# Optimization experiments

Measured on AMD Instinct MI355X. Metric: run time of the kernel, lower is better.

Reference implementation:

```python
import jax, jax.numpy as jnp
import numpy as np

D_MODEL = 256
NUM_HEADS = 8
DIM_HEAD = D_MODEL // NUM_HEADS
EPS = 1e-6
MASK_BIAS = -1.0e9


def setup_inputs() -> dict:
    key = jax.random.key(0)
    ks = jax.random.split(key, 10)
    B, S = 2, 4096
    x = jax.random.normal(ks[0], (B, S, D_MODEL), dtype=jnp.float32)
    pad_mask = jnp.zeros((B, S), dtype=jnp.float32)  # 1.0 => padded position
    scale = 1.0 / np.sqrt(D_MODEL)
    Wq = jax.random.normal(ks[1], (D_MODEL, D_MODEL), dtype=jnp.float32) * scale
    bq = jnp.zeros((D_MODEL,), dtype=jnp.float32)
    Wk = jax.random.normal(ks[2], (D_MODEL, D_MODEL), dtype=jnp.float32) * scale
    bk = jnp.zeros((D_MODEL,), dtype=jnp.float32)
    Wv = jax.random.normal(ks[3], (D_MODEL, D_MODEL), dtype=jnp.float32) * scale
    bv = jnp.zeros((D_MODEL,), dtype=jnp.float32)
    gamma = jnp.ones((D_MODEL,), dtype=jnp.float32)
    beta = jnp.zeros((D_MODEL,), dtype=jnp.float32)
    return {"x": x, "pad_mask": pad_mask, "Wq": Wq, "bq": bq, "Wk": Wk,
            "bk": bk, "Wv": Wv, "bv": bv, "gamma": gamma, "beta": beta}


def _layer_norm(h, gamma, beta):
    mu = jnp.mean(h, axis=-1, keepdims=True)
    var = jnp.mean(jnp.square(h - mu), axis=-1, keepdims=True)
    return gamma * (h - mu) * jax.lax.rsqrt(var + EPS) + beta


def reference(x, pad_mask, Wq, bq, Wk, bk, Wv, bv, gamma, beta):
    B, S, D = x.shape
    q = x @ Wq + bq  # [B,S,D]
    k = x @ Wk + bk
    v = x @ Wv + bv
    # split heads: [B,S,D] -> [B,H,S,Dh]
    def split(t):
        return t.reshape(B, S, NUM_HEADS, DIM_HEAD).transpose(0, 2, 1, 3)
    qh, kh, vh = split(q), split(k), split(v)
    w = jnp.einsum("bhqd,bhkd->bhqk", qh, kh)  # [B,H,S,S]
    # faithful to source: mask added BEFORE the 1/sqrt(dim_head) scaling
    w = w + pad_mask[:, None, None, :] * MASK_BIAS
    w = w / jnp.sqrt(jnp.float32(DIM_HEAD))
    attn = jax.nn.softmax(w, axis=-1)
    # dropout is identity at inference
    out = jnp.einsum("bhqk,bhkd->bhqd", attn, vh)  # [B,H,S,Dh]
    out = out.transpose(0, 2, 1, 3).reshape(B, S, D)
    return _layer_norm(out + x, gamma, beta)
```

## Files before the change

kernel.cpp:

```cpp
#include <hip/hip_runtime.h>
#include <hip/hip_bf16.h>

#define D_MODEL 256
#define NUM_HEADS 8
#define DIM_HEAD 32
#define SEQ 4096
#define BATCH 2
#define NROWS (BATCH * SEQ)
#define LN_EPS 1e-6f
#define MASK_BIAS -1.0e9f
#define SCALE 0.17677669529663687f
#define LOG2E 1.4426950408889634f
#define QSCALE (SCALE * LOG2E)

typedef __attribute__((ext_vector_type(8))) short short8;
typedef __attribute__((ext_vector_type(4))) float f32x4;

static __device__ __forceinline__ unsigned short f2b(float f) {
    union { __hip_bfloat16 b; unsigned short u; } cv;
    cv.b = __float2bfloat16(f);
    return cv.u;
}
static __device__ __forceinline__ unsigned int pk_bf16(float lo, float hi) {
    union { __hip_bfloat162 v; unsigned int u; } cv;
    cv.v = __float22bfloat162_rn(make_float2(lo, hi));
    return cv.u;
}
static __device__ __forceinline__ float exp2_raw(float x) {
#if __has_builtin(__builtin_amdgcn_exp2f)
    return __builtin_amdgcn_exp2f(x);
#else
    float r;
    asm volatile("v_exp_f32 %0, %1" : "=v"(r) : "v"(x));
    return r;
#endif
}
static __device__ __forceinline__ void load_lds16(const void* g, void* l) {
    __builtin_amdgcn_global_load_lds(
        (const __attribute__((address_space(1))) unsigned int*)g,
        (__attribute__((address_space(3))) unsigned int*)l, 16, 0, 0);
}

__global__ __launch_bounds__(256) void prep_kernel(
    const float* __restrict__ Wq, const float* __restrict__ Wk,
    const float* __restrict__ Wv,
    const float* __restrict__ bq, const float* __restrict__ bk,
    const float* __restrict__ bv,
    const float* __restrict__ pad,
    unsigned short* __restrict__ Wt, float* __restrict__ biasc,
    float* __restrict__ T2)
{
    const int blk = blockIdx.x;
    const int t = threadIdx.x;
    if (blk < 768) {
        const int w = blk >> 8;
        const int k = blk & 255;
        const float* W = (w == 0) ? Wq : (w == 1) ? Wk : Wv;
        Wt[(size_t)(w * 256 + t) * 256 + k] = f2b(W[(size_t)k * 256 + t]);
        if (k == 0) {
            const float* bb = (w == 0) ? bq : (w == 1) ? bk : bv;
            biasc[w * 256 + t] = bb[t];
        }
    } else {
        const int i = (blk - 768) * 256 + t;
        T2[i] = pad[i] * (MASK_BIAS * SCALE * LOG2E);
    }
}

__global__ __launch_bounds__(256) void qkv_mfma_kernel(
    const float* __restrict__ x, const unsigned short* __restrict__ Wt,
    const float* __restrict__ biasc,
    unsigned short* __restrict__ Qh, unsigned short* __restrict__ Kh,
    unsigned short* __restrict__ Vt)
{
    const int lane = threadIdx.x & 63;
    const int wid  = threadIdx.x >> 6;
    const int c    = lane & 15;
    const int quad = lane >> 4;

    const int r0 = (blockIdx.x >> 3) * 64 + wid * 16;
    const int n0 = (blockIdx.x & 7) * 96;

    f32x4 acc[6];
    float bias[6];
    #pragma unroll
    for (int t = 0; t < 6; t++) {
        acc[t] = (f32x4){0.f, 0.f, 0.f, 0.f};
        bias[t] = biasc[n0 + 16 * t + c];
    }

    const float* xp0 = x + (size_t)(r0 + c) * D_MODEL + quad * 8;
    const unsigned short* wp0 = Wt + (size_t)(n0 + c) * 256 + quad * 8;

    for (int k0 = 0; k0 < 256; k0 += 32) {
        const float4 a0 = *(const float4*)(xp0 + k0);
        const float4 a1 = *(const float4*)(xp0 + k0 + 4);
        union { unsigned int u[4]; short8 s; } af;
        af.u[0] = pk_bf16(a0.x, a0.y);
        af.u[1] = pk_bf16(a0.z, a0.w);
        af.u[2] = pk_bf16(a1.x, a1.y);
        af.u[3] = pk_bf16(a1.z, a1.w);
        #pragma unroll
        for (int t = 0; t < 6; t++) {
            const short8 bf = *(const short8*)(wp0 + (size_t)(16 * t) * 256 + k0);
            acc[t] = __builtin_amdgcn_mfma_f32_16x16x32_bf16(af.s, bf, acc[t], 0, 0, 0);
        }
    }

    #pragma unroll
    for (int t = 0; t < 6; t++) {
        const int col = n0 + 16 * t;
        const int mm  = col >> 8;
        const int dim = (col & 255) + c;
        const int h = dim >> 5, d = dim & 31;
        const int row = r0 + quad * 4;
        const int bb = row >> 12;
        const int s  = row & (SEQ - 1);
        const size_t bh = (size_t)(bb * NUM_HEADS + h);
        float v0 = acc[t][0] + bias[t];
        float v1 = acc[t][1] + bias[t];
        float v2 = acc[t][2] + bias[t];
        float v3 = acc[t][3] + bias[t];
        if (mm == 2) {
            uint2 pk = make_uint2(pk_bf16(v0, v1), pk_bf16(v2, v3));
            *(uint2*)(Vt + (bh * DIM_HEAD + d) * SEQ + s) = pk;
        } else {
            if (mm == 0) {
                v0 *= QSCALE; v1 *= QSCALE; v2 *= QSCALE; v3 *= QSCALE;
            }
            unsigned short* P = (mm == 0 ? Qh : Kh) + (bh * SEQ + s) * DIM_HEAD + d;
            P[0]  = f2b(v0);
            P[32] = f2b(v1);
            P[64] = f2b(v2);
            P[96] = f2b(v3);
        }
    }
}

__global__ __launch_bounds__(256, 2) void attn_mfma_kernel(
    const unsigned short* __restrict__ Qh, const unsigned short* __restrict__ Kh,
    const unsigned short* __restrict__ Vt, const float* __restrict__ T2,
    float* __restrict__ O)
{
    __shared__ __align__(16) unsigned short ldsK[3][64 * 32];
    __shared__ __align__(16) unsigned short ldsV[3][32 * 64];
    __shared__ __align__(16) float          ldsT[3][64];

    const int lane = threadIdx.x & 63;
    const int wid  = threadIdx.x >> 6;
    const int c    = lane & 15;
    const int quad = lane >> 4;

    const int gw = blockIdx.x;
    const int q0 = (gw & 31) * 128;
    const int h  = (gw >> 5) & (NUM_HEADS - 1);
    const int b  = gw >> 8;
    const size_t bh = (size_t)(b * NUM_HEADS + h);

    const int perm = ((c & 12) << 1) | (c & 3);

    const unsigned short* Kb = Kh + bh * SEQ * DIM_HEAD;
    const unsigned short* Vb = Vt + bh * DIM_HEAD * SEQ;
    const float* Tb = T2 + (size_t)b * SEQ;

    const int qrow = q0 + wid * 32;
    const short8 qfA = *(const short8*)(Qh + (bh * SEQ + qrow + c) * DIM_HEAD + quad * 8);
    const short8 qfB = *(const short8*)(Qh + (bh * SEQ + qrow + 16 + c) * DIM_HEAD + quad * 8);

    union { unsigned int u[4]; short8 s; } ones;
    ones.u[0] = ones.u[1] = ones.u[2] = ones.u[3] = 0x3F803F80u;

    const int f0 = ((perm >> 1) ^ (perm >> 3)) & 3;
    const int f1 = (((perm + 4) >> 1) ^ ((perm + 4) >> 3)) & 3;
    const int kA = perm * 32 + ((quad ^ f0) << 3);
    const int kB = (perm + 4) * 32 + ((quad ^ f1) << 3);
    const int g0 = quad ^ (c & 7);
    const int vA0 = c * 64 + (g0 << 3);
    const int vA1 = c * 64 + ((g0 ^ 4) << 3);
    const int vB0 = (16 + c) * 64 + (g0 << 3);
    const int vB1 = (16 + c) * 64 + ((g0 ^ 4) << 3);

    const int skey = (lane >> 2);
    const int sgK  = lane & 3;
    const int sdim = lane >> 3;
    const int sgV  = lane & 7;

    f32x4 oA0 = {0.f,0.f,0.f,0.f}, oA1 = {0.f,0.f,0.f,0.f};
    f32x4 oB0 = {0.f,0.f,0.f,0.f}, oB1 = {0.f,0.f,0.f,0.f};
    f32x4 laccA = {0.f,0.f,0.f,0.f}, laccB = {0.f,0.f,0.f,0.f};

    auto stage = [&](int ch, int pb) {
        const int s0 = ch * 64;
        if (wid < 2) {
            #pragma unroll
            for (int jj = 0; jj < 2; jj++) {
                const int j = wid * 2 + jj;
                const int key = j * 16 + skey;
                const int f = ((key >> 1) ^ (key >> 3)) & 3;
                load_lds16(Kb + (size_t)(s0 + key) * 32 + ((sgK ^ f) << 3),
                           &ldsK[pb][j * 512]);
            }
        } else {
            #pragma unroll
            for (int jj = 0; jj < 2; jj++) {
                const int j = (wid - 2) * 2 + jj;
                const int dim = j * 8 + sdim;
                load_lds16(Vb + (size_t)dim * SEQ + s0 + ((sgV ^ (dim & 7)) << 3),
                           &ldsV[pb][j * 512]);
            }
            if (wid == 3 && lane < 16)
                load_lds16(Tb + s0 + lane * 4, &ldsT[pb][0]);
        }
    };

    auto sub = [&](int pb, int s) {
        const short8 kf0 = *(const short8*)&ldsK[pb][s * 1024 + kA];
        const short8 kf1 = *(const short8*)&ldsK[pb][s * 1024 + kB];
        const short8 vf0 = *(const short8*)&ldsV[pb][s ? vA1 : vA0];
        const short8 vf1 = *(const short8*)&ldsV[pb][s ? vB1 : vB0];
        const float4 t0 = *(const float4*)&ldsT[pb][s * 32 + quad * 8];
        const float4 t1 = *(const float4*)&ldsT[pb][s * 32 + quad * 8 + 4];

        const f32x4 c0 = {t0.x, t0.y, t0.z, t0.w};
        const f32x4 c1 = {t1.x, t1.y, t1.z, t1.w};

        const f32x4 sA0 = __builtin_amdgcn_mfma_f32_16x16x32_bf16(kf0, qfA, c0, 0, 0, 0);
        const f32x4 sA1 = __builtin_amdgcn_mfma_f32_16x16x32_bf16(kf1, qfA, c1, 0, 0, 0);
        const f32x4 sB0 = __builtin_amdgcn_mfma_f32_16x16x32_bf16(kf0, qfB, c0, 0, 0, 0);
        const f32x4 sB1 = __builtin_amdgcn_mfma_f32_16x16x32_bf16(kf1, qfB, c1, 0, 0, 0);

        union { unsigned int u[4]; short8 s8; } pfA, pfB;
        {
            float p0 = exp2_raw(sA0[0]), p1 = exp2_raw(sA0[1]);
            float p2 = exp2_raw(sA0[2]), p3 = exp2_raw(sA0[3]);
            float p4 = exp2_raw(sA1[0]), p5 = exp2_raw(sA1[1]);
            float p6 = exp2_raw(sA1[2]), p7 = exp2_raw(sA1[3]);
            pfA.u[0] = pk_bf16(p0, p1);
            pfA.u[1] = pk_bf16(p2, p3);
            pfA.u[2] = pk_bf16(p4, p5);
            pfA.u[3] = pk_bf16(p6, p7);
        }
        {
            float p0 = exp2_raw(sB0[0]), p1 = exp2_raw(sB0[1]);
            float p2 = exp2_raw(sB0[2]), p3 = exp2_raw(sB0[3]);
            float p4 = exp2_raw(sB1[0]), p5 = exp2_raw(sB1[1]);
            float p6 = exp2_raw(sB1[2]), p7 = exp2_raw(sB1[3]);
            pfB.u[0] = pk_bf16(p0, p1);
            pfB.u[1] = pk_bf16(p2, p3);
            pfB.u[2] = pk_bf16(p4, p5);
            pfB.u[3] = pk_bf16(p6, p7);
        }

        laccA = __builtin_amdgcn_mfma_f32_16x16x32_bf16(ones.s, pfA.s8, laccA, 0, 0, 0);
        laccB = __builtin_amdgcn_mfma_f32_16x16x32_bf16(ones.s, pfB.s8, laccB, 0, 0, 0);
        oA0   = __builtin_amdgcn_mfma_f32_16x16x32_bf16(vf0,   pfA.s8, oA0,   0, 0, 0);
        oA1   = __builtin_amdgcn_mfma_f32_16x16x32_bf16(vf1,   pfA.s8, oA1,   0, 0, 0);
        oB0   = __builtin_amdgcn_mfma_f32_16x16x32_bf16(vf0,   pfB.s8, oB0,   0, 0, 0);
        oB1   = __builtin_amdgcn_mfma_f32_16x16x32_bf16(vf1,   pfB.s8, oB1,   0, 0, 0);
    };

    stage(0, 0);
    stage(1, 1);

    int rb = 0;
    int sb = 2;
    for (int ch = 0; ch < SEQ / 64; ++ch) {
        if (wid == 3)
            asm volatile("s_waitcnt vmcnt(3) lgkmcnt(0)" ::: "memory");
        else
            asm volatile("s_waitcnt vmcnt(2) lgkmcnt(0)" ::: "memory");
        __builtin_amdgcn_s_barrier();
        __builtin_amdgcn_sched_barrier(0);
        stage((ch + 2) & 63, sb);
        sub(rb, 0);
        sub(rb, 1);
        rb = (rb == 2) ? 0 : rb + 1;
        sb = (sb == 2) ? 0 : sb + 1;
    }

    const float invA = 1.0f / laccA[0];
    const float invB = 1.0f / laccB[0];
    float* opA = O + ((size_t)(b * SEQ) + qrow + c) * D_MODEL + h * DIM_HEAD + quad * 4;
    float* opB = O + ((size_t)(b * SEQ) + qrow + 16 + c) * D_MODEL + h * DIM_HEAD + quad * 4;
    *(float4*)opA        = make_float4(oA0[0]*invA, oA0[1]*invA, oA0[2]*invA, oA0[3]*invA);
    *(float4*)(opA + 16) = make_float4(oA1[0]*invA, oA1[1]*invA, oA1[2]*invA, oA1[3]*invA);
    *(float4*)opB        = make_float4(oB0[0]*invB, oB0[1]*invB, oB0[2]*invB, oB0[3]*invB);
    *(float4*)(opB + 16) = make_float4(oB1[0]*invB, oB1[1]*invB, oB1[2]*invB, oB1[3]*invB);
}

__global__ __launch_bounds__(256) void ln_kernel(
    float* AO,
    const float* __restrict__ x,
    const float* __restrict__ gamma, const float* __restrict__ beta)
{
    const int lane = threadIdx.x & 63;
    const int wid  = threadIdx.x >> 6;
    const size_t row = (size_t)blockIdx.x * 4 + wid;

    const float4 a  = ((const float4*)(AO + row * D_MODEL))[lane];
    const float4 xv = ((const float4*)(x + row * D_MODEL))[lane];
    float hv[4];
    hv[0] = a.x + xv.x;
    hv[1] = a.y + xv.y;
    hv[2] = a.z + xv.z;
    hv[3] = a.w + xv.w;

    float s = hv[0] + hv[1] + hv[2] + hv[3];
    #pragma unroll
    for (int off = 32; off > 0; off >>= 1) s += __shfl_xor(s, off, 64);
    const float mu = s * (1.0f / D_MODEL);

    float d0 = hv[0]-mu, d1 = hv[1]-mu, d2 = hv[2]-mu, d3 = hv[3]-mu;
    float ss = d0*d0 + d1*d1 + d2*d2 + d3*d3;
    #pragma unroll
    for (int off = 32; off > 0; off >>= 1) ss += __shfl_xor(ss, off, 64);
    const float rs = rsqrtf(ss * (1.0f / D_MODEL) + LN_EPS);

    const float4 g  = ((const float4*)gamma)[lane];
    const float4 bb = ((const float4*)beta)[lane];
    float4 y;
    y.x = g.x * d0 * rs + bb.x;
    y.y = g.y * d1 * rs + bb.y;
    y.z = g.z * d2 * rs + bb.z;
    y.w = g.w * d3 * rs + bb.w;
    ((float4*)(AO + row * D_MODEL))[lane] = y;
}

extern "C" void kernel_launch(void* const* d_in, const int* in_sizes, int n_in,
                              void* d_out, int out_size, void* d_ws, size_t ws_size,
                              hipStream_t stream)
{
    const float* x     = (const float*)d_in[0];
    const float* pad   = (const float*)d_in[1];
    const float* Wq    = (const float*)d_in[2];
    const float* bq    = (const float*)d_in[3];
    const float* Wk    = (const float*)d_in[4];
    const float* bk    = (const float*)d_in[5];
    const float* Wv    = (const float*)d_in[6];
    const float* bv    = (const float*)d_in[7];
    const float* gamma = (const float*)d_in[8];
    const float* beta  = (const float*)d_in[9];

    const size_t elems = (size_t)NROWS * D_MODEL;
    unsigned short* Qh = (unsigned short*)d_ws;
    unsigned short* Kh = Qh + elems;
    unsigned short* Vt = Kh + elems;
    float* T2 = (float*)(Vt + elems);
    unsigned short* Wt = (unsigned short*)(T2 + NROWS);
    float* biasc = (float*)(Wt + 768 * 256);
    float* AO = (float*)d_out;

    prep_kernel<<<800, 256, 0, stream>>>(Wq, Wk, Wv, bq, bk, bv, pad,
                                         Wt, biasc, T2);
    qkv_mfma_kernel<<<(NROWS / 64) * 8, 256, 0, stream>>>(x, Wt, biasc,
                                                          Qh, Kh, Vt);
    attn_mfma_kernel<<<BATCH * NUM_HEADS * (SEQ / 128), 256, 0, stream>>>(
        Qh, Kh, Vt, T2, AO);
    ln_kernel<<<NROWS / 4, 256, 0, stream>>>(AO, x, gamma, beta);
}
```

Measured before the change: 178.2 us.

## Split attention key chunks across two wave groups and reduce partials through LDS

The attention block grows from 4 to 8 waves. Each pair of waves shares the same 32 query rows but handles a different half of each 64-key chunk, and the two halves' partial outputs and row sums are combined through LDS at the end. The intent is to double the waves in flight per query tile, which hides MFMA and exp latency better and spreads the staging loads over more waves. The cost is a final LDS reduction with extra barriers and higher per-block thread counts, which may limit occupancy.

```diff
diff --git a/kernel.cpp b/kernel.cpp
--- a/kernel.cpp
+++ b/kernel.cpp
@@ -137,17 +137,19 @@
     }
 }
 
-__global__ __launch_bounds__(256, 2) void attn_mfma_kernel(
+__global__ __launch_bounds__(512, 4) void attn_mfma_kernel(
     const unsigned short* __restrict__ Qh, const unsigned short* __restrict__ Kh,
     const unsigned short* __restrict__ Vt, const float* __restrict__ T2,
     float* __restrict__ O)
 {
-    __shared__ __align__(16) unsigned short ldsK[3][64 * 32];
-    __shared__ __align__(16) unsigned short ldsV[3][32 * 64];
-    __shared__ __align__(16) float          ldsT[3][64];
+    __shared__ __align__(16) unsigned char smem[25344];
+    unsigned short* smem_s = (unsigned short*)smem;
+    float* Tf = (float*)(smem + 24576);
 
     const int lane = threadIdx.x & 63;
     const int wid  = threadIdx.x >> 6;
+    const int cwid = wid & 3;
+    const int shalf = wid >> 2;
     const int c    = lane & 15;
     const int quad = lane >> 4;
 
@@ -163,7 +165,7 @@
     const unsigned short* Vb = Vt + bh * DIM_HEAD * SEQ;
     const float* Tb = T2 + (size_t)b * SEQ;
 
-    const int qrow = q0 + wid * 32;
+    const int qrow = q0 + cwid * 32;
     const short8 qfA = *(const short8*)(Qh + (bh * SEQ + qrow + c) * DIM_HEAD + quad * 8);
     const short8 qfB = *(const short8*)(Qh + (bh * SEQ + qrow + 16 + c) * DIM_HEAD + quad * 8);
 
@@ -191,35 +193,29 @@
 
     auto stage = [&](int ch, int pb) {
         const int s0 = ch * 64;
-        if (wid < 2) {
-            #pragma unroll
-            for (int jj = 0; jj < 2; jj++) {
-                const int j = wid * 2 + jj;
-                const int key = j * 16 + skey;
-                const int f = ((key >> 1) ^ (key >> 3)) & 3;
-                load_lds16(Kb + (size_t)(s0 + key) * 32 + ((sgK ^ f) << 3),
-                           &ldsK[pb][j * 512]);
-            }
+        if (wid < 4) {
+            const int j = wid;
+            const int key = j * 16 + skey;
+            const int f = ((key >> 1) ^ (key >> 3)) & 3;
+            load_lds16(Kb + (size_t)(s0 + key) * 32 + ((sgK ^ f) << 3),
+                       &smem_s[pb * 2048 + j * 512]);
         } else {
-            #pragma unroll
-            for (int jj = 0; jj < 2; jj++) {
-                const int j = (wid - 2) * 2 + jj;
-                const int dim = j * 8 + sdim;
-                load_lds16(Vb + (size_t)dim * SEQ + s0 + ((sgV ^ (dim & 7)) << 3),
-                           &ldsV[pb][j * 512]);
-            }
-            if (wid == 3 && lane < 16)
-                load_lds16(Tb + s0 + lane * 4, &ldsT[pb][0]);
+            const int j = wid - 4;
+            const int dim = j * 8 + sdim;
+            load_lds16(Vb + (size_t)dim * SEQ + s0 + ((sgV ^ (dim & 7)) << 3),
+                       &smem_s[6144 + pb * 2048 + j * 512]);
+            if (wid == 7 && lane < 16)
+                load_lds16(Tb + s0 + lane * 4, Tf + pb * 64);
         }
     };
 
     auto sub = [&](int pb, int s) {
-        const short8 kf0 = *(const short8*)&ldsK[pb][s * 1024 + kA];
-        const short8 kf1 = *(const short8*)&ldsK[pb][s * 1024 + kB];
-        const short8 vf0 = *(const short8*)&ldsV[pb][s ? vA1 : vA0];
-        const short8 vf1 = *(const short8*)&ldsV[pb][s ? vB1 : vB0];
-        const float4 t0 = *(const float4*)&ldsT[pb][s * 32 + quad * 8];
-        const float4 t1 = *(const float4*)&ldsT[pb][s * 32 + quad * 8 + 4];
+        const short8 kf0 = *(const short8*)&smem_s[pb * 2048 + s * 1024 + kA];
+        const short8 kf1 = *(const short8*)&smem_s[pb * 2048 + s * 1024 + kB];
+        const short8 vf0 = *(const short8*)&smem_s[6144 + pb * 2048 + (s ? vA1 : vA0)];
+        const short8 vf1 = *(const short8*)&smem_s[6144 + pb * 2048 + (s ? vB1 : vB0)];
+        const float4 t0 = *(const float4*)&Tf[pb * 64 + s * 32 + quad * 8];
+        const float4 t1 = *(const float4*)&Tf[pb * 64 + s * 32 + quad * 8 + 4];
 
         const f32x4 c0 = {t0.x, t0.y, t0.z, t0.w};
         const f32x4 c1 = {t1.x, t1.y, t1.z, t1.w};
@@ -265,27 +261,50 @@
     int rb = 0;
     int sb = 2;
     for (int ch = 0; ch < SEQ / 64; ++ch) {
-        if (wid == 3)
-            asm volatile("s_waitcnt vmcnt(3) lgkmcnt(0)" ::: "memory");
+        if (wid == 7)
+            asm volatile("s_waitcnt vmcnt(2) lgkmcnt(0)" ::: "memory");
         else
-            asm volatile("s_waitcnt vmcnt(2) lgkmcnt(0)" ::: "memory");
+            asm volatile("s_waitcnt vmcnt(1) lgkmcnt(0)" ::: "memory");
         __builtin_amdgcn_s_barrier();
         __builtin_amdgcn_sched_barrier(0);
         stage((ch + 2) & 63, sb);
-        sub(rb, 0);
-        sub(rb, 1);
+        sub(rb, shalf);
         rb = (rb == 2) ? 0 : rb + 1;
         sb = (sb == 2) ? 0 : sb + 1;
     }
 
-    const float invA = 1.0f / laccA[0];
-    const float invB = 1.0f / laccB[0];
-    float* opA = O + ((size_t)(b * SEQ) + qrow + c) * D_MODEL + h * DIM_HEAD + quad * 4;
-    float* opB = O + ((size_t)(b * SEQ) + qrow + 16 + c) * D_MODEL + h * DIM_HEAD + quad * 4;
-    *(float4*)opA        = make_float4(oA0[0]*invA, oA0[1]*invA, oA0[2]*invA, oA0[3]*invA);
-    *(float4*)(opA + 16) = make_float4(oA1[0]*invA, oA1[1]*invA, oA1[2]*invA, oA1[3]*invA);
-    *(float4*)opB        = make_float4(oB0[0]*invB, oB0[1]*invB, oB0[2]*invB, oB0[3]*invB);
-    *(float4*)(opB + 16) = make_float4(oB1[0]*invB, oB1[1]*invB, oB1[2]*invB, oB1[3]*invB);
+    asm volatile("s_waitcnt vmcnt(0) lgkmcnt(0)" ::: "memory");
+    __builtin_amdgcn_s_barrier();
+
+    float* CS = (float*)smem;
+    if (wid >= 4) {
+        const int slot = (((wid - 4) * 64) + lane) * 20;
+        *(f32x4*)&CS[slot + 0]  = oA0;
+        *(f32x4*)&CS[slot + 4]  = oA1;
+        *(f32x4*)&CS[slot + 8]  = oB0;
+        *(f32x4*)&CS[slot + 12] = oB1;
+        CS[slot + 16] = laccA[0];
+        CS[slot + 17] = laccB[0];
+    }
+    asm volatile("s_waitcnt lgkmcnt(0)" ::: "memory");
+    __builtin_amdgcn_s_barrier();
+    if (wid < 4) {
+        const int slot = ((wid * 64) + lane) * 20;
+        const f32x4 pA0 = *(const f32x4*)&CS[slot + 0];
+        const f32x4 pA1 = *(const f32x4*)&CS[slot + 4];
+        const f32x4 pB0 = *(const f32x4*)&CS[slot + 8];
+        const f32x4 pB1 = *(const f32x4*)&CS[slot + 12];
+        const float invA = 1.0f / (laccA[0] + CS[slot + 16]);
+        const float invB = 1.0f / (laccB[0] + CS[slot + 17]);
+        oA0 += pA0; oA1 += pA1; oB0 += pB0; oB1 += pB1;
+
+        float* opA = O + ((size_t)(b * SEQ) + qrow + c) * D_MODEL + h * DIM_HEAD + quad * 4;
+        float* opB = O + ((size_t)(b * SEQ) + qrow + 16 + c) * D_MODEL + h * DIM_HEAD + quad * 4;
+        *(float4*)opA        = make_float4(oA0[0]*invA, oA0[1]*invA, oA0[2]*invA, oA0[3]*invA);
+        *(float4*)(opA + 16) = make_float4(oA1[0]*invA, oA1[1]*invA, oA1[2]*invA, oA1[3]*invA);
+        *(float4*)opB        = make_float4(oB0[0]*invB, oB0[1]*invB, oB0[2]*invB, oB0[3]*invB);
+        *(float4*)(opB + 16) = make_float4(oB1[0]*invB, oB1[1]*invB, oB1[2]*invB, oB1[3]*invB);
+    }
 }
 
 __global__ __launch_bounds__(256) void ln_kernel(
@@ -354,7 +373,7 @@
                                          Wt, biasc, T2);
     qkv_mfma_kernel<<<(NROWS / 64) * 8, 256, 0, stream>>>(x, Wt, biasc,
                                                           Qh, Kh, Vt);
-    attn_mfma_kernel<<<BATCH * NUM_HEADS * (SEQ / 128), 256, 0, stream>>>(
+    attn_mfma_kernel<<<BATCH * NUM_HEADS * (SEQ / 128), 512, 0, stream>>>(
         Qh, Kh, Vt, T2, AO);
     ln_kernel<<<NROWS / 4, 256, 0, stream>>>(AO, x, gamma, beta);
 }
```

Result: no change. 180.9 us (+1.5%).
